# Kernel optimization log

Hardware: AMD Instinct MI355X
Metric: run time of the kernel (lower is better)

Reference implementation:

```python
import jax, jax.numpy as jnp
import numpy as np

H = 256
NUM_CONVS = 4
NUM_GRAPHS = 1024
N_PER_GRAPH = 32
ORDER = 3
NUM_TYPES = 22  # len(utils.BOND_TYPES)
NUM_NOISE_LEVEL = 50
ANNEAL_POWER = 2.0


def _build_graph():
    # Chain molecules extended to order-3 neighbors (mimics extend_graph on a path graph):
    # for |i-j| in [1,ORDER]: edge_order=|i-j|, edge_type = bond type if order 1 else NUM_TYPES+order-1.
    n = N_PER_GRAPH
    i, j = np.meshgrid(np.arange(n), np.arange(n), indexing='ij')
    dist = np.abs(i - j)
    mask = (dist >= 1) & (dist <= ORDER)
    src_l, dst_l, eo = i[mask], j[mask], dist[mask]
    offs = np.arange(NUM_GRAPHS)[:, None] * n
    src = (src_l[None, :] + offs).reshape(-1)
    dst = (dst_l[None, :] + offs).reshape(-1)
    edge_order = np.tile(eo, NUM_GRAPHS)
    rng = np.random.default_rng(0)
    bond_t = rng.integers(1, 5, size=edge_order.shape)
    edge_type = np.where(edge_order == 1, bond_t, NUM_TYPES + edge_order - 1)
    node2graph = np.repeat(np.arange(NUM_GRAPHS), n)
    return src, dst, edge_type, node2graph


def setup_inputs() -> dict:
    key = jax.random.key(0)
    ks = jax.random.split(key, 24)
    src, dst, edge_type, node2graph = _build_graph()
    N, E = node2graph.shape[0], src.shape[0]
    w = lambda k, s: (jax.random.normal(k, s, jnp.float32) * 0.05)
    sigmas = jnp.asarray(np.exp(np.linspace(np.log(10.0), np.log(0.01), NUM_NOISE_LEVEL)), dtype=jnp.float32)
    return {
        'atom_type': jnp.asarray(np.random.default_rng(1).integers(0, 100, N), jnp.int32),
        'edge_index': jnp.asarray(np.stack([src, dst]), jnp.int32),
        'edge_type': jnp.asarray(edge_type, jnp.int32),
        'node2graph': jnp.asarray(node2graph, jnp.int32),
        'noise_level': jax.random.randint(ks[0], (NUM_GRAPHS,), 0, NUM_NOISE_LEVEL, jnp.int32),
        'pos': jax.random.normal(ks[1], (N, 3), jnp.float32) * 3.0,
        'd_noise': jax.random.normal(ks[2], (E, 1), jnp.float32),
        'sigmas': sigmas,
        'node_emb': w(ks[3], (100, H)), 'edge_emb': w(ks[4], (100, H)),
        'in_W1': w(ks[5], (1, H)), 'in_b1': w(ks[6], (H,)),
        'in_W2': w(ks[7], (H, H)), 'in_b2': w(ks[8], (H,)),
        'gin_W1': w(ks[9], (NUM_CONVS, H, H)), 'gin_b1': w(ks[10], (NUM_CONVS, H)),
        'gin_W2': w(ks[11], (NUM_CONVS, H, H)), 'gin_b2': w(ks[12], (NUM_CONVS, H)),
        'out_W1': w(ks[13], (2 * H, H)), 'out_b1': w(ks[14], (H,)),
        'out_W2': w(ks[15], (H, H // 2)), 'out_b2': w(ks[16], (H // 2,)),
        'out_W3': w(ks[17], (H // 2, 1)), 'out_b3': w(ks[18], (1,)),
    }


def reference(atom_type, edge_index, edge_type, node2graph, noise_level,
              pos, d_noise, sigmas, node_emb, edge_emb,
              in_W1, in_b1, in_W2, in_b2,
              gin_W1, gin_b1, gin_W2, gin_b2,
              out_W1, out_b1, out_W2, out_b2, out_W3, out_b3):
    N = pos.shape[0]
    G = noise_level.shape[0]
    row, col = edge_index[0], edge_index[1]
    edge2graph = node2graph[row]                                  # [E]
    d = jnp.linalg.norm(pos[row] - pos[col], axis=-1, keepdims=True)  # [E,1]
    used_sigmas = sigmas[noise_level][edge2graph][:, None]        # [E,1]
    perturbed_d = d + d_noise * used_sigmas
    target = -(perturbed_d - d) / used_sigmas ** 2
    # embeddings + input MLP (Linear-relu-Linear)
    node_attr = node_emb[atom_type]                               # [N,H]
    d_emb = jax.nn.relu(perturbed_d @ in_W1 + in_b1) @ in_W2 + in_b2
    edge_attr = d_emb * edge_emb[edge_type]                       # [E,H]
    # GIN with GINE convs: agg = sum_j relu(x_j + e_ij); out = MLP(x + agg); relu between convs; residual
    x = node_attr
    n_convs = gin_W1.shape[0]
    for k in range(n_convs):
        msg = jax.nn.relu(x[row] + edge_attr)                     # [E,H]
        agg = jax.ops.segment_sum(msg, col, num_segments=N)       # [N,H]
        h = jax.nn.relu((x + agg) @ gin_W1[k] + gin_b1[k]) @ gin_W2[k] + gin_b2[k]
        if k < n_convs - 1:
            h = jax.nn.relu(h)
        x = h + x  # short_cut
    # edge score head
    feat = jnp.concatenate([x[row] * x[col], edge_attr], axis=-1)  # [E,2H]
    s = jax.nn.relu(feat @ out_W1 + out_b1)
    s = jax.nn.relu(s @ out_W2 + out_b2)
    s = s @ out_W3 + out_b3                                       # [E,1]
    scores = (s / used_sigmas).reshape(-1)
    t = target.reshape(-1)
    loss_e = 0.5 * (scores - t) ** 2 * used_sigmas.reshape(-1) ** ANNEAL_POWER
    return jax.ops.segment_sum(loss_e, edge2graph, num_segments=G)  # [G]
```

## Files before the change

### kernel.cpp

```cpp
#include <hip/hip_runtime.h>
#include <math.h>

typedef unsigned int u32;
typedef __attribute__((ext_vector_type(8))) short bf16x8;
typedef __attribute__((ext_vector_type(4))) float f32x4;

#define MFMA16(a,b,c) __builtin_amdgcn_mfma_f32_16x16x32_bf16(a,b,c,0,0,0)

__device__ inline u32 bf16r(float x){
  u32 u = __float_as_uint(x);
  return (u + 0x7fffu + ((u >> 16) & 1u)) >> 16;
}
__device__ inline u32 pack2(float a, float b){ return bf16r(a) | (bf16r(b) << 16); }
__device__ inline uint4 pack8(const float* f){
  uint4 v; v.x = pack2(f[0],f[1]); v.y = pack2(f[2],f[3]);
  v.z = pack2(f[4],f[5]); v.w = pack2(f[6],f[7]); return v;
}
__device__ inline float bf2f(short s){ return __uint_as_float(((u32)(unsigned short)s) << 16); }

__device__ __forceinline__ void gload_lds16(const void* g, void* l){
  __builtin_amdgcn_global_load_lds((const __attribute__((address_space(1))) unsigned int*)g,
                                   (__attribute__((address_space(3))) unsigned int*)l,
                                   16, 0, 0);
}

__device__ __forceinline__ int frag_off(int f, int quad){
  return (f>>1)*64 + (f&1)*32 + ((quad ^ ((f>>1)&3))*8);
}

__device__ __forceinline__ int xg(int g, int r){ return g ^ ((r ^ (g>>3)) & 7); }

__global__ void k_cvtAll(const float* __restrict__ inW2, const float* __restrict__ gW1,
                         const float* __restrict__ gW2, const float* __restrict__ oW1,
                         const float* __restrict__ oW2,
                         short* __restrict__ w2t, short* __restrict__ gw1t,
                         short* __restrict__ gw2t, short* __restrict__ ow1t,
                         short* __restrict__ ow2t){
  int gidx = blockIdx.x*256 + threadIdx.x;
  const float* src; short* dst; int t, K8, Nf;
  if (gidx < 8192)      { src = inW2; dst = w2t; t = gidx; K8 = 32; Nf = 256; }
  else if (gidx < 40960){ int r = gidx-8192;  int c = r>>13; t = r&8191;
                          src = gW1 + (size_t)c*65536; dst = gw1t + (size_t)c*65536; K8 = 32; Nf = 256; }
  else if (gidx < 73728){ int r = gidx-40960; int c = r>>13; t = r&8191;
                          src = gW2 + (size_t)c*65536; dst = gw2t + (size_t)c*65536; K8 = 32; Nf = 256; }
  else if (gidx < 90112){ t = gidx-73728; src = oW1; dst = ow1t; K8 = 64; Nf = 256; }
  else if (gidx < 94208){ t = gidx-90112; src = oW2; dst = ow2t; K8 = 32; Nf = 128; }
  else return;
  int f = t / K8, c = t - f*K8;
  float v[8];
  #pragma unroll
  for (int j=0;j<8;j++) v[j] = src[(size_t)(c*8+j)*Nf + f];
  ((uint4*)dst)[t] = pack8(v);
}

__global__ void k_pre(const int* __restrict__ ei, const int* __restrict__ n2g,
                      const int* __restrict__ nl, const float* __restrict__ sigmas,
                      const float* __restrict__ pos, const float* __restrict__ dn, int E,
                      float* __restrict__ pd, int* __restrict__ cnt, int* __restrict__ inlist){
  int e = blockIdx.x*256 + threadIdx.x;
  if (e >= E) return;
  int r = ei[e], c = ei[E+e];
  float sg = sigmas[nl[n2g[r]]];
  float dx = pos[3*r]-pos[3*c], dy = pos[3*r+1]-pos[3*c+1], dz = pos[3*r+2]-pos[3*c+2];
  float d = sqrtf(dx*dx + dy*dy + dz*dz);
  pd[e] = d + dn[e]*sg;
  int slot = atomicAdd(&cnt[c], 1);
  if (slot < 8) inlist[c*8 + slot] = e;
}

__global__ __launch_bounds__(256) void k_attr(
    const float* __restrict__ pd, const float* __restrict__ W1, const float* __restrict__ b1,
    const short* __restrict__ W2t, const float* __restrict__ b2,
    const int* __restrict__ etype, const float* __restrict__ eemb,
    short* __restrict__ attr, int E)
{
  int tid = threadIdx.x;
  int base = blockIdx.x*64;
  int wv = tid>>6, lane = tid&63, quad = lane>>4, l15 = lane&15;
  float pdv[4];
  #pragma unroll
  for (int nt=0;nt<4;nt++) pdv[nt] = pd[base + nt*16 + l15];
  f32x4 acc[4][4];
  #pragma unroll
  for (int mt=0;mt<4;mt++) for (int nt=0;nt<4;nt++) acc[mt][nt] = (f32x4)0.f;
  #pragma unroll
  for (int s=0; s<8; s++){
    int k0 = s*32 + quad*8;
    float4 w1a = *(const float4*)(W1 + k0), w1b = *(const float4*)(W1 + k0 + 4);
    float4 b1a = *(const float4*)(b1 + k0), b1b = *(const float4*)(b1 + k0 + 4);
    bf16x8 a[4], b[4];
    #pragma unroll
    for (int mt=0;mt<4;mt++){
      int f = (wv*4+mt)*16 + l15;
      a[mt] = *(const bf16x8*)(W2t + (size_t)f*256 + k0);
    }
    #pragma unroll
    for (int nt=0;nt<4;nt++){
      float p = pdv[nt];
      float f[8] = {fmaxf(p*w1a.x+b1a.x,0.f), fmaxf(p*w1a.y+b1a.y,0.f),
                    fmaxf(p*w1a.z+b1a.z,0.f), fmaxf(p*w1a.w+b1a.w,0.f),
                    fmaxf(p*w1b.x+b1b.x,0.f), fmaxf(p*w1b.y+b1b.y,0.f),
                    fmaxf(p*w1b.z+b1b.z,0.f), fmaxf(p*w1b.w+b1b.w,0.f)};
      uint4 u = pack8(f);
      b[nt] = *(bf16x8*)&u;
    }
    #pragma unroll
    for (int mt=0;mt<4;mt++)
      #pragma unroll
      for (int nt=0;nt<4;nt++)
        acc[mt][nt] = MFMA16(a[mt], b[nt], acc[mt][nt]);
  }
  #pragma unroll
  for (int nt=0;nt<4;nt++){
    int e = base + nt*16 + l15;
    int et = etype[e];
    #pragma unroll
    for (int mt=0;mt<4;mt++){
      int f0 = (wv*4+mt)*16 + quad*4;
      float4 bb = *(const float4*)(b2 + f0);
      float4 em = *(const float4*)(eemb + (size_t)et*256 + f0);
      float v0 = (acc[mt][nt][0]+bb.x)*em.x, v1 = (acc[mt][nt][1]+bb.y)*em.y;
      float v2 = (acc[mt][nt][2]+bb.z)*em.z, v3 = (acc[mt][nt][3]+bb.w)*em.w;
      uint2 v; v.x = pack2(v0,v1); v.y = pack2(v2,v3);
      *(uint2*)(attr + (size_t)e*256 + f0) = v;
    }
  }
}

#define EPG 180
__global__ __launch_bounds__(256,1) void k_conv4(
    const int* __restrict__ at, const float* __restrict__ nemb,
    const short* __restrict__ attrS, const int* __restrict__ ei,
    const int* __restrict__ cnt, const int* __restrict__ inlist,
    const short* __restrict__ gw1t, const float* __restrict__ gb1,
    const short* __restrict__ gw2t, const float* __restrict__ gb2,
    short* __restrict__ xF)
{
  __shared__ float xls[32*256];
  __shared__ uint4 AlsV[32*32];
  __shared__ uint4 attrLV[EPG*32];
  short* Als = (short*)AlsV;
  short* T1  = Als;
  short* attrL = (short*)attrLV;
  int tid = threadIdx.x;
  int nbase = blockIdx.x*32;
  int ebase = blockIdx.x*EPG;
  int wv = tid>>6, lane = tid&63, quad = lane>>4, l15 = lane&15;
  int jl = tid>>3, ch = tid&7;
  {
    const char* src = (const char*)(attrS + (size_t)ebase*256) + lane*16;
    char* dst = (char*)attrLV;
    #pragma unroll
    for (int i=0; i<23; i++){
      int r = i*4 + wv;
      if (r < 90) gload_lds16(src + r*1024, dst + r*1024);
    }
  }
  int deg, eid[8], rl[8];
  {
    int j = nbase + jl;
    deg = min(cnt[j], 8);
    #pragma unroll
    for (int s=0;s<8;s++){
      eid[s] = (s < deg) ? (inlist[j*8 + s] - ebase) : 0;
      rl[s]  = (s < deg) ? (ei[ebase + eid[s]] - nbase) : 0;
    }
  }
  {
    int a = at[nbase + jl];
    const float4* src = (const float4*)nemb + (size_t)a*64 + ch*8;
    float* xrow = xls + jl*256;
    #pragma unroll
    for (int q=0;q<8;q++)
      *(float4*)(xrow + (xg(ch*8+q, jl)<<2)) = src[q];
  }
  __syncthreads();
  for (int c=0; c<4; c++){
    const short* W1t = gw1t + (size_t)c*65536;
    const short* W2t = gw2t + (size_t)c*65536;
    const float* b1 = gb1 + c*256;
    const float* b2 = gb2 + c*256;
    {
      float f[32];
      const float* xrow = xls + jl*256;
      #pragma unroll
      for (int q=0;q<8;q++){
        float4 v = *(const float4*)(xrow + (xg(ch*8+q, jl)<<2));
        f[q*4]=v.x; f[q*4+1]=v.y; f[q*4+2]=v.z; f[q*4+3]=v.w;
      }
      for (int sIt=0; sIt<deg; sIt++){
        int r = rl[sIt];
        const float* xr = xls + r*256;
        const short* ar = attrL + eid[sIt]*256 + ch*32;
        #pragma unroll
        for (int q=0;q<8;q++){
          float4 xv = *(const float4*)(xr + (xg(ch*8+q, r)<<2));
          u32 lo = *(const u32*)(ar + q*4);
          u32 hi = *(const u32*)(ar + q*4 + 2);
          f[q*4]   += fmaxf(xv.x + __uint_as_float(lo<<16), 0.f);
          f[q*4+1] += fmaxf(xv.y + __uint_as_float(lo&0xffff0000u), 0.f);
          f[q*4+2] += fmaxf(xv.z + __uint_as_float(hi<<16), 0.f);
          f[q*4+3] += fmaxf(xv.w + __uint_as_float(hi&0xffff0000u), 0.f);
        }
      }
      #pragma unroll
      for (int qq=0;qq<4;qq++)
        *(uint4*)(Als + jl*256 + (((ch*4+qq) ^ (jl&7))*8)) = pack8(f + qq*8);
    }
    __syncthreads();
    f32x4 acc[4][2];
    #pragma unroll
    for (int mt=0;mt<4;mt++) for (int nt=0;nt<2;nt++) acc[mt][nt] = (f32x4)0.f;
    #pragma unroll
    for (int s=0; s<8; s++){
      bf16x8 a[4], b[2];
      #pragma unroll
      for (int mt=0;mt<4;mt++)
        a[mt] = *(const bf16x8*)(W1t + (size_t)((wv*4+mt)*16 + l15)*256 + s*32 + quad*8);
      #pragma unroll
      for (int nt=0;nt<2;nt++){
        int n = nt*16 + l15; int cc = s*4 + quad;
        b[nt] = *(const bf16x8*)(Als + n*256 + ((cc ^ (n&7))*8));
      }
      #pragma unroll
      for (int mt=0;mt<4;mt++)
        #pragma unroll
        for (int nt=0;nt<2;nt++)
          acc[mt][nt] = MFMA16(a[mt], b[nt], acc[mt][nt]);
    }
    __syncthreads();
    #pragma unroll
    for (int mt=0;mt<4;mt++){
      int f0 = (wv*4+mt)*16 + quad*4;
      float4 bb = *(const float4*)(b1 + f0);
      int cg = f0 >> 3, off = (quad&1)*4;
      #pragma unroll
      for (int nt=0;nt<2;nt++){
        int n = nt*16 + l15;
        float v0 = fmaxf(acc[mt][nt][0]+bb.x,0.f), v1 = fmaxf(acc[mt][nt][1]+bb.y,0.f);
        float v2 = fmaxf(acc[mt][nt][2]+bb.z,0.f), v3 = fmaxf(acc[mt][nt][3]+bb.w,0.f);
        uint2 v; v.x = pack2(v0,v1); v.y = pack2(v2,v3);
        *(uint2*)(T1 + n*256 + ((cg ^ (n&7))*8) + off) = v;
      }
    }
    __syncthreads();
    f32x4 acc2[4][2];
    #pragma unroll
    for (int mt=0;mt<4;mt++) for (int nt=0;nt<2;nt++) acc2[mt][nt] = (f32x4)0.f;
    #pragma unroll
    for (int s=0; s<8; s++){
      bf16x8 a[4], b[2];
      #pragma unroll
      for (int mt=0;mt<4;mt++)
        a[mt] = *(const bf16x8*)(W2t + (size_t)((wv*4+mt)*16 + l15)*256 + s*32 + quad*8);
      #pragma unroll
      for (int nt=0;nt<2;nt++){
        int n = nt*16 + l15; int cc = s*4 + quad;
        b[nt] = *(const bf16x8*)(T1 + n*256 + ((cc ^ (n&7))*8));
      }
      #pragma unroll
      for (int mt=0;mt<4;mt++)
        #pragma unroll
        for (int nt=0;nt<2;nt++)
          acc2[mt][nt] = MFMA16(a[mt], b[nt], acc2[mt][nt]);
    }
    #pragma unroll
    for (int mt=0;mt<4;mt++){
      int f0 = (wv*4+mt)*16 + quad*4;
      float4 bb = *(const float4*)(b2 + f0);
      int g = f0 >> 2;
      #pragma unroll
      for (int nt=0;nt<2;nt++){
        int n = nt*16 + l15;
        float* px = xls + n*256 + (xg(g, n)<<2);
        float4 xv = *(float4*)px;
        float h0 = acc2[mt][nt][0]+bb.x, h1 = acc2[mt][nt][1]+bb.y;
        float h2 = acc2[mt][nt][2]+bb.z, h3 = acc2[mt][nt][3]+bb.w;
        if (c < 3){ h0=fmaxf(h0,0.f); h1=fmaxf(h1,0.f); h2=fmaxf(h2,0.f); h3=fmaxf(h3,0.f); }
        xv.x += h0; xv.y += h1; xv.z += h2; xv.w += h3;
        *(float4*)px = xv;
      }
    }
    __syncthreads();
  }
  {
    const float* xrow = xls + jl*256;
    float f[32];
    #pragma unroll
    for (int q=0;q<8;q++){
      float4 v = *(const float4*)(xrow + (xg(ch*8+q, jl)<<2));
      f[q*4]=v.x; f[q*4+1]=v.y; f[q*4+2]=v.z; f[q*4+3]=v.w;
    }
    #pragma unroll
    for (int qq=0;qq<4;qq++)
      *(uint4*)(xF + (size_t)(nbase+jl)*256 + ch*32 + qq*8) = pack8(f + qq*8);
  }
}

__global__ __launch_bounds__(256,2) void k_head(
    const short* __restrict__ xF, const short* __restrict__ attrS,
    const int* __restrict__ ei,
    const short* __restrict__ W1t, const float* __restrict__ ob1,
    const short* __restrict__ W2t, const float* __restrict__ ob2,
    const float* __restrict__ W3, const float* __restrict__ ob3,
    const float* __restrict__ dnoise, const int* __restrict__ n2g,
    float* __restrict__ out, int E, int G)
{
  __shared__ uint4 BlsV[16*256];
  __shared__ float Sedge[64];
  __shared__ float part[4];
  short* Bls = (short*)BlsV;
  short* T   = (short*)BlsV;
  int tid = threadIdx.x;
  int base = blockIdx.x*64;
  int wv = tid>>6, lane = tid&63, quad = lane>>4, l15 = lane&15;
  if (tid < 64) Sedge[tid] = 0.f;
  if (tid < 4) part[tid] = 0.f;
  {
    int g = wv*64 + lane;
    int p = g>>3, hi = (g>>2)&1, cs = g&3;
    int n = p*2 + hi, cc = cs ^ (p&3);
    const short* srcb = attrS + (size_t)(base+n)*256 + cc*8;
    #pragma unroll
    for (int s=8; s<16; s++)
      gload_lds16(srcb + (s-8)*32, (char*)Bls + (size_t)s*4096 + wv*1024);
  }
  {
    int g = tid;
    int p = g>>3, hi = (g>>2)&1, cs = g&3;
    int n = p*2 + hi, cc = cs ^ (p&3);
    int rr = ei[base+n], rc = ei[E+base+n];
    const short* xr = xF + (size_t)rr*256 + cc*8;
    const short* xc = xF + (size_t)rc*256 + cc*8;
    #pragma unroll
    for (int s=0; s<8; s++){
      bf16x8 va = *(const bf16x8*)(xr + s*32);
      bf16x8 vb = *(const bf16x8*)(xc + s*32);
      float f[8];
      #pragma unroll
      for (int j=0;j<8;j++) f[j] = bf2f(va[j])*bf2f(vb[j]);
      *(uint4*)(Bls + (size_t)s*2048 + g*8) = pack8(f);
    }
  }
  __syncthreads();
  f32x4 acc[4][4];
  #pragma unroll
  for (int mt=0;mt<4;mt++) for (int nt=0;nt<4;nt++) acc[mt][nt] = (f32x4)0.f;
  #pragma unroll
  for (int s=0; s<16; s++){
    bf16x8 a[4], b[4];
    #pragma unroll
    for (int mt=0;mt<4;mt++)
      a[mt] = *(const bf16x8*)(W1t + (size_t)((wv*4+mt)*16 + l15)*512 + s*32 + quad*8);
    #pragma unroll
    for (int nt=0;nt<4;nt++)
      b[nt] = *(const bf16x8*)(Bls + (size_t)s*2048 + frag_off(nt*16 + l15, quad));
    #pragma unroll
    for (int mt=0;mt<4;mt++)
      #pragma unroll
      for (int nt=0;nt<4;nt++)
        acc[mt][nt] = MFMA16(a[mt], b[nt], acc[mt][nt]);
  }
  __syncthreads();
  #pragma unroll
  for (int mt=0;mt<4;mt++){
    int f0 = (wv*4+mt)*16 + quad*4;
    float4 bb = *(const float4*)(ob1 + f0);
    int c = f0 >> 3, off = (quad&1)*4;
    #pragma unroll
    for (int nt=0;nt<4;nt++){
      int n = nt*16 + l15;
      float v0 = fmaxf(acc[mt][nt][0]+bb.x,0.f), v1 = fmaxf(acc[mt][nt][1]+bb.y,0.f);
      float v2 = fmaxf(acc[mt][nt][2]+bb.z,0.f), v3 = fmaxf(acc[mt][nt][3]+bb.w,0.f);
      uint2 v; v.x = pack2(v0,v1); v.y = pack2(v2,v3);
      *(uint2*)(T + n*256 + ((c ^ (n&7))*8) + off) = v;
    }
  }
  __syncthreads();
  f32x4 acc2[2][4];
  #pragma unroll
  for (int mt=0;mt<2;mt++) for (int nt=0;nt<4;nt++) acc2[mt][nt] = (f32x4)0.f;
  #pragma unroll
  for (int s=0; s<8; s++){
    bf16x8 a[2], b[4];
    #pragma unroll
    for (int mt=0;mt<2;mt++)
      a[mt] = *(const bf16x8*)(W2t + (size_t)((wv*2+mt)*16 + l15)*256 + s*32 + quad*8);
    #pragma unroll
    for (int nt=0;nt<4;nt++){
      int n = nt*16 + l15; int cc = s*4 + quad;
      b[nt] = *(const bf16x8*)(T + n*256 + ((cc ^ (n&7))*8));
    }
    #pragma unroll
    for (int mt=0;mt<2;mt++)
      #pragma unroll
      for (int nt=0;nt<4;nt++)
        acc2[mt][nt] = MFMA16(a[mt], b[nt], acc2[mt][nt]);
  }
  float4 b2v[2], w3v[2];
  #pragma unroll
  for (int mt=0;mt<2;mt++){
    int f0 = (wv*2+mt)*16 + quad*4;
    b2v[mt] = *(const float4*)(ob2 + f0);
    w3v[mt] = *(const float4*)(W3 + f0);
  }
  #pragma unroll
  for (int nt=0;nt<4;nt++){
    float p = 0.f;
    #pragma unroll
    for (int mt=0;mt<2;mt++){
      p += fmaxf(acc2[mt][nt][0]+b2v[mt].x,0.f)*w3v[mt].x;
      p += fmaxf(acc2[mt][nt][1]+b2v[mt].y,0.f)*w3v[mt].y;
      p += fmaxf(acc2[mt][nt][2]+b2v[mt].z,0.f)*w3v[mt].z;
      p += fmaxf(acc2[mt][nt][3]+b2v[mt].w,0.f)*w3v[mt].w;
    }
    p += __shfl_xor(p, 16);
    p += __shfl_xor(p, 32);
    if (lane < 16) atomicAdd(&Sedge[nt*16 + l15], p);
  }
  __syncthreads();
  int gbase = n2g[ei[base]];
  if (tid < 64){
    int e = base + tid;
    float sv = Sedge[tid] + ob3[0] + dnoise[e];
    float l = 0.5f*sv*sv;
    int g = n2g[ei[e]] - gbase;
    atomicAdd(&part[g & 3], l);
  }
  __syncthreads();
  if (tid < 2 && (gbase + tid) < G)
    atomicAdd(&out[gbase + tid], part[tid]);
}

static inline size_t alignup(size_t v){ return (v + 255) & ~(size_t)255; }

extern "C" void kernel_launch(void* const* d_in, const int* in_sizes, int n_in,
                              void* d_out, int out_size, void* d_ws, size_t ws_size,
                              hipStream_t stream) {
  const int*   at    = (const int*)  d_in[0];
  const int*   ei    = (const int*)  d_in[1];
  const int*   etype = (const int*)  d_in[2];
  const int*   n2g   = (const int*)  d_in[3];
  const int*   nl    = (const int*)  d_in[4];
  const float* pos   = (const float*)d_in[5];
  const float* dnoi  = (const float*)d_in[6];
  const float* sig   = (const float*)d_in[7];
  const float* nemb  = (const float*)d_in[8];
  const float* eemb  = (const float*)d_in[9];
  const float* inW1  = (const float*)d_in[10];
  const float* inb1  = (const float*)d_in[11];
  const float* inW2  = (const float*)d_in[12];
  const float* inb2  = (const float*)d_in[13];
  const float* gW1   = (const float*)d_in[14];
  const float* gb1   = (const float*)d_in[15];
  const float* gW2   = (const float*)d_in[16];
  const float* gb2   = (const float*)d_in[17];
  const float* oW1   = (const float*)d_in[18];
  const float* ob1   = (const float*)d_in[19];
  const float* oW2   = (const float*)d_in[20];
  const float* ob2   = (const float*)d_in[21];
  const float* oW3   = (const float*)d_in[22];
  const float* ob3   = (const float*)d_in[23];
  float* out = (float*)d_out;

  const int N = in_sizes[0];
  const int E = in_sizes[2];
  const int G = in_sizes[4];
  const int H = 256;

  char* w = (char*)d_ws;
  size_t off = 0;
  size_t o_attr  = off; off = alignup(off + (size_t)E*H*2);
  size_t o_xF    = off; off = alignup(off + (size_t)N*H*2);
  size_t o_pd    = off; off = alignup(off + (size_t)E*4);
  size_t o_cnt   = off; off = alignup(off + (size_t)N*4);
  size_t o_inl   = off; off = alignup(off + (size_t)N*8*4);
  size_t o_w2t   = off; off = alignup(off + (size_t)H*H*2);
  size_t o_gw1t  = off; off = alignup(off + (size_t)4*H*H*2);
  size_t o_gw2t  = off; off = alignup(off + (size_t)4*H*H*2);
  size_t o_ow1t  = off; off = alignup(off + (size_t)H*2*H*2);
  size_t o_ow2t  = off; off = alignup(off + (size_t)(H/2)*H*2);
  (void)ws_size; (void)n_in; (void)out_size;

  short* attrS = (short*)(w + o_attr);
  short* xF    = (short*)(w + o_xF);
  float* pd    = (float*)(w + o_pd);
  int*   cnt   = (int*)  (w + o_cnt);
  int*   inl   = (int*)  (w + o_inl);
  short* w2t   = (short*)(w + o_w2t);
  short* gw1t  = (short*)(w + o_gw1t);
  short* gw2t  = (short*)(w + o_gw2t);
  short* ow1t  = (short*)(w + o_ow1t);
  short* ow2t  = (short*)(w + o_ow2t);

  hipMemsetAsync(cnt, 0, (size_t)N*4, stream);
  hipMemsetAsync(out, 0, (size_t)G*4, stream);

  k_cvtAll<<<368, 256, 0, stream>>>(inW2, gW1, gW2, oW1, oW2,
                                    w2t, gw1t, gw2t, ow1t, ow2t);

  k_pre<<<(E+255)/256, 256, 0, stream>>>(ei, n2g, nl, sig, pos, dnoi, E, pd, cnt, inl);
  k_attr<<<E/64, 256, 0, stream>>>(pd, inW1, inb1, w2t, inb2, etype, eemb, attrS, E);

  k_conv4<<<G, 256, 0, stream>>>(at, nemb, attrS, ei, cnt, inl,
                                 gw1t, gb1, gw2t, gb2, xF);

  k_head<<<E/64, 256, 0, stream>>>(xF, attrS, ei, ow1t, ob1, ow2t, ob2,
                                   oW3, ob3, dnoi, n2g, out, E, G);
}
```

Before: 594.1 us.

## Widen conv kernel to 1024 threads per graph with separate T1 buffer

The per-graph GIN conv kernel now runs with 16 wavefronts instead of 4. Each thread aggregates 8 features instead of 32, and each wave computes one 16-row M-tile instead of four. A separate LDS buffer for the first MLP layer output removes one barrier between the two GEMMs. This adds latency hiding and parallelism per CU, at the cost of more LDS, a larger block needing more resources, and each wave issuing its own weight loads with less reuse per wave.

```diff
diff --git a/kernel.cpp b/kernel.cpp
--- a/kernel.cpp
+++ b/kernel.cpp
@@ -128,7 +128,7 @@
 }
 
 #define EPG 180
-__global__ __launch_bounds__(256,1) void k_conv4(
+__global__ __launch_bounds__(1024,1) void k_conv4(
     const int* __restrict__ at, const float* __restrict__ nemb,
     const short* __restrict__ attrS, const int* __restrict__ ei,
     const int* __restrict__ cnt, const int* __restrict__ inlist,
@@ -138,21 +138,22 @@
 {
   __shared__ float xls[32*256];
   __shared__ uint4 AlsV[32*32];
+  __shared__ uint4 T1V [32*32];
   __shared__ uint4 attrLV[EPG*32];
   short* Als = (short*)AlsV;
-  short* T1  = Als;
+  short* T1  = (short*)T1V;
   short* attrL = (short*)attrLV;
   int tid = threadIdx.x;
   int nbase = blockIdx.x*32;
   int ebase = blockIdx.x*EPG;
   int wv = tid>>6, lane = tid&63, quad = lane>>4, l15 = lane&15;
-  int jl = tid>>3, ch = tid&7;
+  int jl = tid>>5, ch = tid&31;
   {
     const char* src = (const char*)(attrS + (size_t)ebase*256) + lane*16;
     char* dst = (char*)attrLV;
     #pragma unroll
-    for (int i=0; i<23; i++){
-      int r = i*4 + wv;
+    for (int i=0; i<6; i++){
+      int r = i*16 + wv;
       if (r < 90) gload_lds16(src + r*1024, dst + r*1024);
     }
   }
@@ -168,11 +169,11 @@
   }
   {
     int a = at[nbase + jl];
-    const float4* src = (const float4*)nemb + (size_t)a*64 + ch*8;
+    const float4* src = (const float4*)nemb + (size_t)a*64 + ch*2;
     float* xrow = xls + jl*256;
     #pragma unroll
-    for (int q=0;q<8;q++)
-      *(float4*)(xrow + (xg(ch*8+q, jl)<<2)) = src[q];
+    for (int q=0;q<2;q++)
+      *(float4*)(xrow + (xg(ch*2+q, jl)<<2)) = src[q];
   }
   __syncthreads();
   for (int c=0; c<4; c++){
@@ -181,92 +182,71 @@
     const float* b1 = gb1 + c*256;
     const float* b2 = gb2 + c*256;
     {
-      float f[32];
+      float f[8];
       const float* xrow = xls + jl*256;
       #pragma unroll
-      for (int q=0;q<8;q++){
-        float4 v = *(const float4*)(xrow + (xg(ch*8+q, jl)<<2));
+      for (int q=0;q<2;q++){
+        float4 v = *(const float4*)(xrow + (xg(ch*2+q, jl)<<2));
         f[q*4]=v.x; f[q*4+1]=v.y; f[q*4+2]=v.z; f[q*4+3]=v.w;
       }
       for (int sIt=0; sIt<deg; sIt++){
         int r = rl[sIt];
         const float* xr = xls + r*256;
-        const short* ar = attrL + eid[sIt]*256 + ch*32;
+        uint4 a4 = *(const uint4*)(attrL + eid[sIt]*256 + ch*8);
         #pragma unroll
-        for (int q=0;q<8;q++){
-          float4 xv = *(const float4*)(xr + (xg(ch*8+q, r)<<2));
-          u32 lo = *(const u32*)(ar + q*4);
-          u32 hi = *(const u32*)(ar + q*4 + 2);
+        for (int q=0;q<2;q++){
+          float4 xv = *(const float4*)(xr + (xg(ch*2+q, r)<<2));
+          u32 lo = (q==0) ? a4.x : a4.z;
+          u32 hi = (q==0) ? a4.y : a4.w;
           f[q*4]   += fmaxf(xv.x + __uint_as_float(lo<<16), 0.f);
           f[q*4+1] += fmaxf(xv.y + __uint_as_float(lo&0xffff0000u), 0.f);
           f[q*4+2] += fmaxf(xv.z + __uint_as_float(hi<<16), 0.f);
           f[q*4+3] += fmaxf(xv.w + __uint_as_float(hi&0xffff0000u), 0.f);
         }
       }
-      #pragma unroll
-      for (int qq=0;qq<4;qq++)
-        *(uint4*)(Als + jl*256 + (((ch*4+qq) ^ (jl&7))*8)) = pack8(f + qq*8);
+      *(uint4*)(Als + jl*256 + ((ch ^ (jl&7))*8)) = pack8(f);
     }
     __syncthreads();
-    f32x4 acc[4][2];
-    #pragma unroll
-    for (int mt=0;mt<4;mt++) for (int nt=0;nt<2;nt++) acc[mt][nt] = (f32x4)0.f;
+    f32x4 acc[2];
+    acc[0] = (f32x4)0.f; acc[1] = (f32x4)0.f;
     #pragma unroll
     for (int s=0; s<8; s++){
-      bf16x8 a[4], b[2];
-      #pragma unroll
-      for (int mt=0;mt<4;mt++)
-        a[mt] = *(const bf16x8*)(W1t + (size_t)((wv*4+mt)*16 + l15)*256 + s*32 + quad*8);
+      bf16x8 a = *(const bf16x8*)(W1t + (size_t)(wv*16 + l15)*256 + s*32 + quad*8);
       #pragma unroll
       for (int nt=0;nt<2;nt++){
         int n = nt*16 + l15; int cc = s*4 + quad;
-        b[nt] = *(const bf16x8*)(Als + n*256 + ((cc ^ (n&7))*8));
-      }
-      #pragma unroll
-      for (int mt=0;mt<4;mt++)
-        #pragma unroll
-        for (int nt=0;nt<2;nt++)
-          acc[mt][nt] = MFMA16(a[mt], b[nt], acc[mt][nt]);
-    }
-    __syncthreads();
-    #pragma unroll
-    for (int mt=0;mt<4;mt++){
-      int f0 = (wv*4+mt)*16 + quad*4;
+        bf16x8 b = *(const bf16x8*)(Als + n*256 + ((cc ^ (n&7))*8));
+        acc[nt] = MFMA16(a, b, acc[nt]);
+      }
+    }
+    {
+      int f0 = wv*16 + quad*4;
       float4 bb = *(const float4*)(b1 + f0);
       int cg = f0 >> 3, off = (quad&1)*4;
       #pragma unroll
       for (int nt=0;nt<2;nt++){
         int n = nt*16 + l15;
-        float v0 = fmaxf(acc[mt][nt][0]+bb.x,0.f), v1 = fmaxf(acc[mt][nt][1]+bb.y,0.f);
-        float v2 = fmaxf(acc[mt][nt][2]+bb.z,0.f), v3 = fmaxf(acc[mt][nt][3]+bb.w,0.f);
+        float v0 = fmaxf(acc[nt][0]+bb.x,0.f), v1 = fmaxf(acc[nt][1]+bb.y,0.f);
+        float v2 = fmaxf(acc[nt][2]+bb.z,0.f), v3 = fmaxf(acc[nt][3]+bb.w,0.f);
         uint2 v; v.x = pack2(v0,v1); v.y = pack2(v2,v3);
         *(uint2*)(T1 + n*256 + ((cg ^ (n&7))*8) + off) = v;
       }
     }
     __syncthreads();
-    f32x4 acc2[4][2];
-    #pragma unroll
-    for (int mt=0;mt<4;mt++) for (int nt=0;nt<2;nt++) acc2[mt][nt] = (f32x4)0.f;
+    f32x4 acc2[2];
+    acc2[0] = (f32x4)0.f; acc2[1] = (f32x4)0.f;
     #pragma unroll
     for (int s=0; s<8; s++){
-      bf16x8 a[4], b[2];
-      #pragma unroll
-      for (int mt=0;mt<4;mt++)
-        a[mt] = *(const bf16x8*)(W2t + (size_t)((wv*4+mt)*16 + l15)*256 + s*32 + quad*8);
+      bf16x8 a = *(const bf16x8*)(W2t + (size_t)(wv*16 + l15)*256 + s*32 + quad*8);
       #pragma unroll
       for (int nt=0;nt<2;nt++){
         int n = nt*16 + l15; int cc = s*4 + quad;
-        b[nt] = *(const bf16x8*)(T1 + n*256 + ((cc ^ (n&7))*8));
-      }
-      #pragma unroll
-      for (int mt=0;mt<4;mt++)
-        #pragma unroll
-        for (int nt=0;nt<2;nt++)
-          acc2[mt][nt] = MFMA16(a[mt], b[nt], acc2[mt][nt]);
-    }
-    #pragma unroll
-    for (int mt=0;mt<4;mt++){
-      int f0 = (wv*4+mt)*16 + quad*4;
+        bf16x8 b = *(const bf16x8*)(T1 + n*256 + ((cc ^ (n&7))*8));
+        acc2[nt] = MFMA16(a, b, acc2[nt]);
+      }
+    }
+    {
+      int f0 = wv*16 + quad*4;
       float4 bb = *(const float4*)(b2 + f0);
       int g = f0 >> 2;
       #pragma unroll
@@ -274,8 +254,8 @@
         int n = nt*16 + l15;
         float* px = xls + n*256 + (xg(g, n)<<2);
         float4 xv = *(float4*)px;
-        float h0 = acc2[mt][nt][0]+bb.x, h1 = acc2[mt][nt][1]+bb.y;
-        float h2 = acc2[mt][nt][2]+bb.z, h3 = acc2[mt][nt][3]+bb.w;
+        float h0 = acc2[nt][0]+bb.x, h1 = acc2[nt][1]+bb.y;
+        float h2 = acc2[nt][2]+bb.z, h3 = acc2[nt][3]+bb.w;
         if (c < 3){ h0=fmaxf(h0,0.f); h1=fmaxf(h1,0.f); h2=fmaxf(h2,0.f); h3=fmaxf(h3,0.f); }
         xv.x += h0; xv.y += h1; xv.z += h2; xv.w += h3;
         *(float4*)px = xv;
@@ -285,15 +265,13 @@
   }
   {
     const float* xrow = xls + jl*256;
-    float f[32];
-    #pragma unroll
-    for (int q=0;q<8;q++){
-      float4 v = *(const float4*)(xrow + (xg(ch*8+q, jl)<<2));
+    float f[8];
+    #pragma unroll
+    for (int q=0;q<2;q++){
+      float4 v = *(const float4*)(xrow + (xg(ch*2+q, jl)<<2));
       f[q*4]=v.x; f[q*4+1]=v.y; f[q*4+2]=v.z; f[q*4+3]=v.w;
     }
-    #pragma unroll
-    for (int qq=0;qq<4;qq++)
-      *(uint4*)(xF + (size_t)(nbase+jl)*256 + ch*32 + qq*8) = pack8(f + qq*8);
+    *(uint4*)(xF + (size_t)(nbase+jl)*256 + ch*8) = pack8(f);
   }
 }
 
@@ -502,8 +480,8 @@
   k_pre<<<(E+255)/256, 256, 0, stream>>>(ei, n2g, nl, sig, pos, dnoi, E, pd, cnt, inl);
   k_attr<<<E/64, 256, 0, stream>>>(pd, inW1, inb1, w2t, inb2, etype, eemb, attrS, E);
 
-  k_conv4<<<G, 256, 0, stream>>>(at, nemb, attrS, ei, cnt, inl,
-                                 gw1t, gb1, gw2t, gb2, xF);
+  k_conv4<<<G, 1024, 0, stream>>>(at, nemb, attrS, ei, cnt, inl,
+                                  gw1t, gb1, gw2t, gb2, xF);
 
   k_head<<<E/64, 256, 0, stream>>>(xF, attrS, ei, ow1t, ob1, ow2t, ob2,
                                    oW3, ob3, dnoi, n2g, out, E, G);
```

Result: faster. 535.0 us (-9.9%).
